# Optimization experiments

Hardware: AMD Instinct MI355X
Metric: run time of the kernel (lower is better)

The kernel has to match this reference:

```python
import jax, jax.numpy as jnp
import numpy as np

N_EMBED = 384
NUM_HEADS = 6
HEAD_SIZE = 64
B, T = 128, 256


def setup_inputs() -> dict:
    key = jax.random.key(0)
    ks = jax.random.split(key, 6)
    x = jax.random.normal(ks[0], (B, T, N_EMBED), dtype=jnp.float32)
    s = 0.02
    Wq = jax.random.normal(ks[1], (NUM_HEADS, N_EMBED, HEAD_SIZE), dtype=jnp.float32) * s
    Wk = jax.random.normal(ks[2], (NUM_HEADS, N_EMBED, HEAD_SIZE), dtype=jnp.float32) * s
    Wv = jax.random.normal(ks[3], (NUM_HEADS, N_EMBED, HEAD_SIZE), dtype=jnp.float32) * s
    Wp = jax.random.normal(ks[4], (NUM_HEADS * HEAD_SIZE, N_EMBED), dtype=jnp.float32) * s
    bp = jnp.zeros((N_EMBED,), dtype=jnp.float32)
    return {"x": x, "Wq": Wq, "Wk": Wk, "Wv": Wv, "Wp": Wp, "bp": bp}


def reference(x, Wq, Wk, Wv, Wp, bp):
    # x: [B,T,C]; Wq/Wk/Wv: [H,C,hs]; Wp: [H*hs, C]
    Bx, Tx, C = x.shape
    q = jnp.einsum('btc,hcd->bhtd', x, Wq)
    k = jnp.einsum('btc,hcd->bhtd', x, Wk)
    v = jnp.einsum('btc,hcd->bhtd', x, Wv)
    scale = HEAD_SIZE ** (-0.5)
    scores = jnp.einsum('bhtd,bhsd->bhts', q, k) * scale  # [B,H,T,T]
    causal = jnp.tril(jnp.ones((Tx, Tx), dtype=bool))
    scores = jnp.where(causal, scores, -jnp.inf)
    attn = jax.nn.softmax(scores, axis=-1)
    # dropout is identity in eval mode
    out = jnp.einsum('bhts,bhsd->bhtd', attn, v)  # [B,H,T,hs]
    out = out.transpose(0, 2, 1, 3).reshape(Bx, Tx, NUM_HEADS * HEAD_SIZE)
    return out @ Wp + bp
```

## Files before the change

### kernel.cpp

```cpp
#include <hip/hip_runtime.h>
#include <hip/hip_bf16.h>

#define C_DIM 384
#define H_NUM 6
#define HS    64
#define B_DIM 128
#define T_DIM 256
#define NROWS (B_DIM * T_DIM)

typedef unsigned short u16;
typedef unsigned int u32;
typedef short bf16x8 __attribute__((ext_vector_type(8)));
typedef float floatx4 __attribute__((ext_vector_type(4)));

__device__ __forceinline__ u16 f2b(float f) {
  __hip_bfloat16 h = __float2bfloat16(f);
  u16 u;
  __builtin_memcpy(&u, &h, 2);
  return u;
}
__device__ __forceinline__ void gload_lds16(const void* g, void* lds) {
  __builtin_amdgcn_global_load_lds(
      (const __attribute__((address_space(1))) u32*)g,
      (__attribute__((address_space(3))) u32*)lds, 16, 0, 0);
}

__global__ __launch_bounds__(256) void prep_kernel(
    const float* __restrict__ x, const float* __restrict__ Wq,
    const float* __restrict__ Wk, const float* __restrict__ Wv,
    const float* __restrict__ Wp, u16* __restrict__ xb,
    u16* __restrict__ Wh, u16* __restrict__ Wpt) {
  const int bid = blockIdx.x;
  const int tid = threadIdx.x;
  if (bid < 6144) {
    const int i = bid * 256 + tid;
    const int row = (i * 8) / C_DIM;
    const int c8 = (i * 8) % C_DIM;
    const float* p = x + (size_t)i * 8;
    const float4 f0 = *(const float4*)p;
    const float4 f1 = *(const float4*)(p + 4);
    bf16x8 pk;
    pk[0] = (short)f2b(f0.x); pk[1] = (short)f2b(f0.y);
    pk[2] = (short)f2b(f0.z); pk[3] = (short)f2b(f0.w);
    pk[4] = (short)f2b(f1.x); pk[5] = (short)f2b(f1.y);
    pk[6] = (short)f2b(f1.z); pk[7] = (short)f2b(f1.w);
    const int cd = c8 ^ ((row & 7) << 3);
    ((bf16x8*)xb)[(row * C_DIM + cd) >> 3] = pk;
  } else {
    const int idx = (bid - 6144) * 256 + tid;
    const int WHN = H_NUM * 192 * C_DIM;
    if (idx < WHN) {
      int h = idx / (192 * C_DIM);
      int rem = idx % (192 * C_DIM);
      int r = rem / C_DIM, c = rem % C_DIM;
      int tz = r >> 6, d = r & 63;
      const int cs = c ^ ((r & 7) << 3);
      const float* W = (tz == 0) ? Wq : (tz == 1) ? Wk : Wv;
      Wh[idx] = f2b(W[((size_t)h * C_DIM + cs) * HS + d]);
    } else {
      int j = idx - WHN;
      int n = j / C_DIM, c = j % C_DIM;
      const int cs = c ^ ((n & 7) << 3);
      Wpt[j] = f2b(Wp[cs * C_DIM + n]);
    }
  }
}

#define AS0_OFF 0
#define AS1_OFF 16384
#define BS0_OFF 32768
#define BS1_OFF 45056
#define QS_OFF  0
#define KLS_OFF 16384
#define VTS_OFF 32768
#define PLS_OFF 49152

template <bool DIAG>
__device__ __forceinline__ void attn_chunk_f(int c, int mt, int lane, int ln,
                                             int qd, const bf16x8* qf,
                                             const u16* smem, u16* Pw,
                                             floatx4* oacc, float* lsum) {
  floatx4 sacc[4];
#pragma unroll
  for (int st = 0; st < 4; ++st) {
    sacc[st] = floatx4{0.f, 0.f, 0.f, 0.f};
#pragma unroll
    for (int kc = 0; kc < 2; ++kc) {
      bf16x8 kf = *(const bf16x8*)&smem[KLS_OFF + ((c * 4 + st) * 2 + kc) * 512 +
                                        lane * 8];
      sacc[st] =
          __builtin_amdgcn_mfma_f32_16x16x32_bf16(qf[kc], kf, sacc[st], 0, 0, 0);
    }
  }
#pragma unroll
  for (int st = 0; st < 4; ++st) {
#pragma unroll
    for (int r = 0; r < 4; ++r) {
      const float sv = sacc[st][r] * 0.125f;
      float p = __expf(sv);
      if (DIAG) {
        const bool ok = (c * 64 + st * 16 + ln) <= (mt * 16 + qd * 4 + r);
        p = ok ? p : 0.f;
      }
      lsum[r] += p;
      Pw[(qd * 4 + r) * 72 + st * 16 + ln] = f2b(p);
    }
  }
#pragma unroll
  for (int kc2 = 0; kc2 < 2; ++kc2) {
    bf16x8 pf = *(const bf16x8*)&Pw[ln * 72 + kc2 * 32 + qd * 8];
#pragma unroll
    for (int dt = 0; dt < 4; ++dt) {
      bf16x8 vf = *(const bf16x8*)&smem[VTS_OFF + (dt * 16 + ln) * 256 +
                                        ((c * 64 + kc2 * 32 + qd * 8) ^
                                         ((ln & 7) << 3))];
      oacc[dt] =
          __builtin_amdgcn_mfma_f32_16x16x32_bf16(pf, vf, oacc[dt], 0, 0, 0);
    }
  }
}

__global__ __launch_bounds__(512) void qkv_attn_fused(
    const u16* __restrict__ xb, const u16* __restrict__ Wh,
    u16* __restrict__ y) {
  __shared__ __align__(16) u16 smem[58368];
  const int b = blockIdx.x;
  const int h = blockIdx.y;
  const u16* a_rows = xb + (size_t)b * 256 * C_DIM;
  const u16* wbase = Wh + (size_t)h * 192 * C_DIM;

  const int tid = threadIdx.x;
  const int lane = tid & 63;
  const int w = tid >> 6;
  const int lr = lane >> 3;
  const int lkc = (lane & 7) * 8;
  const int qd = lane >> 4;
  const int ln = lane & 15;
  const int sx = (ln & 7) << 3;
  const int wm = (w >> 1) * 64;
  const int wn = (w & 1) * 96;

  floatx4 acc[4][6];
#pragma unroll
  for (int i = 0; i < 4; ++i)
#pragma unroll
    for (int j = 0; j < 6; ++j) acc[i][j] = floatx4{0.f, 0.f, 0.f, 0.f};

#pragma unroll
  for (int s = 0; s < 4; ++s) {
    const int rbase = (s * 8 + w) * 8;
    gload_lds16(a_rows + (size_t)(rbase + lr) * C_DIM + lkc,
                smem + AS0_OFF + rbase * 64);
  }
#pragma unroll
  for (int s = 0; s < 3; ++s) {
    const int rbase = (s * 8 + w) * 8;
    gload_lds16(wbase + (size_t)(rbase + lr) * C_DIM + lkc,
                smem + BS0_OFF + rbase * 64);
  }

  for (int kb = 0; kb < 6; ++kb) {
    const int pa = (kb & 1) ? AS1_OFF : AS0_OFF;
    const int pb = (kb & 1) ? BS1_OFF : BS0_OFF;
    if (kb < 5) {
      const int qa = (kb & 1) ? AS0_OFF : AS1_OFF;
      const int qb = (kb & 1) ? BS0_OFF : BS1_OFF;
      const int k0 = (kb + 1) * 64;
#pragma unroll
      for (int s = 0; s < 4; ++s) {
        const int rbase = (s * 8 + w) * 8;
        gload_lds16(a_rows + (size_t)(rbase + lr) * C_DIM + k0 + lkc,
                    smem + qa + rbase * 64);
      }
#pragma unroll
      for (int s = 0; s < 3; ++s) {
        const int rbase = (s * 8 + w) * 8;
        gload_lds16(wbase + (size_t)(rbase + lr) * C_DIM + k0 + lkc,
                    smem + qb + rbase * 64);
      }
      asm volatile("s_waitcnt vmcnt(7)" ::: "memory");
    } else {
      asm volatile("s_waitcnt vmcnt(0)" ::: "memory");
    }
    __builtin_amdgcn_s_barrier();
    __builtin_amdgcn_sched_barrier(0);

#pragma unroll
    for (int kk = 0; kk < 2; ++kk) {
      bf16x8 af[4], bf[6];
#pragma unroll
      for (int mt = 0; mt < 4; ++mt)
        af[mt] = *(const bf16x8*)&smem[pa + (wm + mt * 16 + ln) * 64 +
                                       ((kk * 32 + qd * 8) ^ sx)];
#pragma unroll
      for (int nt = 0; nt < 6; ++nt)
        bf[nt] = *(const bf16x8*)&smem[pb + (wn + nt * 16 + ln) * 64 +
                                       ((kk * 32 + qd * 8) ^ sx)];
#pragma unroll
      for (int mt = 0; mt < 4; ++mt)
#pragma unroll
        for (int nt = 0; nt < 6; ++nt)
          acc[mt][nt] = __builtin_amdgcn_mfma_f32_16x16x32_bf16(
              af[mt], bf[nt], acc[mt][nt], 0, 0, 0);
    }
    __builtin_amdgcn_sched_barrier(0);
    __builtin_amdgcn_s_barrier();
  }

#pragma unroll
  for (int nt = 0; nt < 6; ++nt) {
    const int c0 = wn + nt * 16;
#pragma unroll
    for (int mt = 0; mt < 4; ++mt) {
#pragma unroll
      for (int r = 0; r < 4; ++r) {
        const int t = wm + mt * 16 + qd * 4 + r;
        const u16 val = f2b(acc[mt][nt][r]);
        if (c0 < 64) {
          smem[QS_OFF + t * 64 + c0 + ln] = val;
        } else if (c0 < 128) {
          const int d = c0 - 64 + ln;
          smem[KLS_OFF + ((t >> 4) << 10) + ((d >> 5) << 9) +
               (((d >> 3) & 3) << 7) + ((t & 15) << 3) + (d & 7)] = val;
        } else {
          const int dv = c0 - 128 + ln;
          smem[VTS_OFF + dv * 256 + (t ^ ((dv & 7) << 3))] = val;
        }
      }
    }
  }
  __syncthreads();

  u16* Pw = smem + PLS_OFF + w * 1152;
#pragma unroll
  for (int i = 0; i < 2; ++i) {
    const int mt = i ? (15 - w) : w;
    bf16x8 qf[2];
#pragma unroll
    for (int kc = 0; kc < 2; ++kc)
      qf[kc] = *(const bf16x8*)&smem[QS_OFF + (mt * 16 + ln) * 64 + kc * 32 +
                                     qd * 8];

    floatx4 oacc[4];
    float lsum[4];
#pragma unroll
    for (int dt = 0; dt < 4; ++dt) oacc[dt] = floatx4{0.f, 0.f, 0.f, 0.f};
#pragma unroll
    for (int r = 0; r < 4; ++r) lsum[r] = 0.f;

    const int cmax = mt >> 2;
    for (int c = 0; c < cmax; ++c)
      attn_chunk_f<false>(c, mt, lane, ln, qd, qf, smem, Pw, oacc, lsum);
    attn_chunk_f<true>(cmax, mt, lane, ln, qd, qf, smem, Pw, oacc, lsum);

#pragma unroll
    for (int off = 1; off < 16; off <<= 1)
#pragma unroll
      for (int r = 0; r < 4; ++r) lsum[r] += __shfl_xor(lsum[r], off);

#pragma unroll
    for (int r = 0; r < 4; ++r) {
      const float inv = 1.f / lsum[r];
      const int t = mt * 16 + qd * 4 + r;
      const int sy = (t & 7) << 3;
      u16* yo = y + ((size_t)b * T_DIM + t) * C_DIM + h * HS;
#pragma unroll
      for (int dt = 0; dt < 4; ++dt)
        yo[(dt * 16 + ln) ^ sy] = f2b(oacc[dt][r] * inv);
    }
  }
}

#define PAS0 0
#define PAS1 8192
#define PBS0 16384
#define PBS1 24576

__global__ __launch_bounds__(256) void proj_gemm(
    const u16* __restrict__ yb, const u16* __restrict__ Wpt,
    const float* __restrict__ bp, float* __restrict__ out) {
  __shared__ __align__(16) u16 smem[33792];
  const int row0 = blockIdx.x * 128;
  const int n0 = blockIdx.y * 128;
  const u16* a_rows = yb + (size_t)row0 * C_DIM;
  const u16* bt_rows = Wpt + (size_t)n0 * C_DIM;

  const int tid = threadIdx.x;
  const int lane = tid & 63;
  const int w = tid >> 6;
  const int lr = lane >> 3;
  const int lkc = (lane & 7) * 8;
  const int qd = lane >> 4;
  const int ln = lane & 15;
  const int sx = (ln & 7) << 3;
  const int mw = (w >> 1) * 64;
  const int nw = (w & 1) * 64;

  floatx4 acc[4][4];
#pragma unroll
  for (int i = 0; i < 4; ++i)
#pragma unroll
    for (int j = 0; j < 4; ++j) acc[i][j] = floatx4{0.f, 0.f, 0.f, 0.f};

#pragma unroll
  for (int s = 0; s < 4; ++s) {
    const int rbase = (s * 4 + w) * 8;
    gload_lds16(a_rows + (size_t)(rbase + lr) * C_DIM + lkc,
                smem + PAS0 + rbase * 64);
    gload_lds16(bt_rows + (size_t)(rbase + lr) * C_DIM + lkc,
                smem + PBS0 + rbase * 64);
  }

  for (int kb = 0; kb < 6; ++kb) {
    const int pa = (kb & 1) ? PAS1 : PAS0;
    const int pb = (kb & 1) ? PBS1 : PBS0;
    if (kb < 5) {
      const int qa = (kb & 1) ? PAS0 : PAS1;
      const int qb = (kb & 1) ? PBS0 : PBS1;
      const int k0 = (kb + 1) * 64;
#pragma unroll
      for (int s = 0; s < 4; ++s) {
        const int rbase = (s * 4 + w) * 8;
        gload_lds16(a_rows + (size_t)(rbase + lr) * C_DIM + k0 + lkc,
                    smem + qa + rbase * 64);
        gload_lds16(bt_rows + (size_t)(rbase + lr) * C_DIM + k0 + lkc,
                    smem + qb + rbase * 64);
      }
      asm volatile("s_waitcnt vmcnt(8)" ::: "memory");
    } else {
      asm volatile("s_waitcnt vmcnt(0)" ::: "memory");
    }
    __builtin_amdgcn_s_barrier();
    __builtin_amdgcn_sched_barrier(0);

#pragma unroll
    for (int kk = 0; kk < 2; ++kk) {
      bf16x8 af[4], bf[4];
#pragma unroll
      for (int mt = 0; mt < 4; ++mt)
        af[mt] = *(const bf16x8*)&smem[pa + (mw + mt * 16 + ln) * 64 +
                                       ((kk * 32 + qd * 8) ^ sx)];
#pragma unroll
      for (int nt = 0; nt < 4; ++nt)
        bf[nt] = *(const bf16x8*)&smem[pb + (nw + nt * 16 + ln) * 64 +
                                       ((kk * 32 + qd * 8) ^ sx)];
#pragma unroll
      for (int mt = 0; mt < 4; ++mt)
#pragma unroll
        for (int nt = 0; nt < 4; ++nt)
          acc[mt][nt] = __builtin_amdgcn_mfma_f32_16x16x32_bf16(
              af[mt], bf[nt], acc[mt][nt], 0, 0, 0);
    }
    __builtin_amdgcn_sched_barrier(0);
    __builtin_amdgcn_s_barrier();
  }

  float* Osf = (float*)smem;
#pragma unroll
  for (int nt = 0; nt < 4; ++nt) {
#pragma unroll
    for (int mt = 0; mt < 4; ++mt) {
#pragma unroll
      for (int r = 0; r < 4; ++r) {
        Osf[(mw + mt * 16 + qd * 4 + r) * 132 + nw + nt * 16 + ln] =
            acc[mt][nt][r];
      }
    }
  }
  __syncthreads();
#pragma unroll
  for (int it = 0; it < 16; ++it) {
    const int idx = it * 1024 + tid * 4;
    const int lrow = idx >> 7, lcol = idx & 127;
    const float4 o = *(const float4*)&Osf[lrow * 132 + lcol];
    const float4 bb = *(const float4*)&bp[n0 + lcol];
    const float4 res{o.x + bb.x, o.y + bb.y, o.z + bb.z, o.w + bb.w};
    *(float4*)&out[(size_t)(row0 + lrow) * C_DIM + n0 + lcol] = res;
  }
}

extern "C" void kernel_launch(void* const* d_in, const int* in_sizes, int n_in,
                              void* d_out, int out_size, void* d_ws, size_t ws_size,
                              hipStream_t stream) {
  const float* x  = (const float*)d_in[0];
  const float* Wq = (const float*)d_in[1];
  const float* Wk = (const float*)d_in[2];
  const float* Wv = (const float*)d_in[3];
  const float* Wp = (const float*)d_in[4];
  const float* bp = (const float*)d_in[5];
  float* out = (float*)d_out;

  const size_t n_x = (size_t)NROWS * C_DIM;

  u16* Wh  = (u16*)d_ws;
  u16* Wpt = Wh + (size_t)H_NUM * 192 * C_DIM;
  u16* xb  = Wpt + C_DIM * C_DIM;
  u16* y   = xb + n_x;

  prep_kernel<<<6144 + 2304, 256, 0, stream>>>(x, Wq, Wk, Wv, Wp, xb, Wh, Wpt);
  qkv_attn_fused<<<dim3(B_DIM, H_NUM), 512, 0, stream>>>(xb, Wh, y);
  proj_gemm<<<dim3(NROWS / 128, 3), 256, 0, stream>>>(y, Wpt, bp, out);
}
```

Measured before the change: 182.8 us.

## Fuse output projection into attention kernel via last-head-arrives counter

Removes the separate projection GEMM launch. Each attention block increments a per-batch atomic counter after writing its head output, and the last of the six head blocks for a batch computes the full 256x384 projection for that batch, including the bias add, writing floats directly without LDS staging. This saves a kernel launch and lets projection overlap with other batches' attention, but the projection work is done serially by only 128 blocks at the tail and output stores are uncoalesced per-lane scalar writes.

```diff
diff --git a/kernel.cpp b/kernel.cpp
--- a/kernel.cpp
+++ b/kernel.cpp
@@ -29,7 +29,7 @@
     const float* __restrict__ x, const float* __restrict__ Wq,
     const float* __restrict__ Wk, const float* __restrict__ Wv,
     const float* __restrict__ Wp, u16* __restrict__ xb,
-    u16* __restrict__ Wh, u16* __restrict__ Wpt) {
+    u16* __restrict__ Wh, u16* __restrict__ Wpt, u32* __restrict__ cnt) {
   const int bid = blockIdx.x;
   const int tid = threadIdx.x;
   if (bid < 6144) {
@@ -48,6 +48,7 @@
     ((bf16x8*)xb)[(row * C_DIM + cd) >> 3] = pk;
   } else {
     const int idx = (bid - 6144) * 256 + tid;
+    if (bid == 6144 && tid < B_DIM) cnt[tid] = 0;
     const int WHN = H_NUM * 192 * C_DIM;
     if (idx < WHN) {
       int h = idx / (192 * C_DIM);
@@ -74,6 +75,11 @@
 #define KLS_OFF 16384
 #define VTS_OFF 32768
 #define PLS_OFF 49152
+#define PA0_OFF 0
+#define PA1_OFF 16384
+#define PB0_OFF 32768
+#define PB1_OFF 40960
+#define FLAG_OFF 49152
 
 template <bool DIAG>
 __device__ __forceinline__ void attn_chunk_f(int c, int mt, int lane, int ln,
@@ -122,7 +128,8 @@
 
 __global__ __launch_bounds__(512) void qkv_attn_fused(
     const u16* __restrict__ xb, const u16* __restrict__ Wh,
-    u16* __restrict__ y) {
+    const u16* __restrict__ Wpt, const float* __restrict__ bp,
+    u16* __restrict__ y, float* __restrict__ out, u32* __restrict__ cnt) {
   __shared__ __align__(16) u16 smem[58368];
   const int b = blockIdx.x;
   const int h = blockIdx.y;
@@ -269,113 +276,105 @@
         yo[(dt * 16 + ln) ^ sy] = f2b(oacc[dt][r] * inv);
     }
   }
-}
-
-#define PAS0 0
-#define PAS1 8192
-#define PBS0 16384
-#define PBS1 24576
-
-__global__ __launch_bounds__(256) void proj_gemm(
-    const u16* __restrict__ yb, const u16* __restrict__ Wpt,
-    const float* __restrict__ bp, float* __restrict__ out) {
-  __shared__ __align__(16) u16 smem[33792];
-  const int row0 = blockIdx.x * 128;
-  const int n0 = blockIdx.y * 128;
-  const u16* a_rows = yb + (size_t)row0 * C_DIM;
-  const u16* bt_rows = Wpt + (size_t)n0 * C_DIM;
-
-  const int tid = threadIdx.x;
-  const int lane = tid & 63;
-  const int w = tid >> 6;
-  const int lr = lane >> 3;
-  const int lkc = (lane & 7) * 8;
-  const int qd = lane >> 4;
-  const int ln = lane & 15;
-  const int sx = (ln & 7) << 3;
-  const int mw = (w >> 1) * 64;
-  const int nw = (w & 1) * 64;
-
-  floatx4 acc[4][4];
-#pragma unroll
-  for (int i = 0; i < 4; ++i)
-#pragma unroll
-    for (int j = 0; j < 4; ++j) acc[i][j] = floatx4{0.f, 0.f, 0.f, 0.f};
-
-#pragma unroll
-  for (int s = 0; s < 4; ++s) {
-    const int rbase = (s * 4 + w) * 8;
-    gload_lds16(a_rows + (size_t)(rbase + lr) * C_DIM + lkc,
-                smem + PAS0 + rbase * 64);
-    gload_lds16(bt_rows + (size_t)(rbase + lr) * C_DIM + lkc,
-                smem + PBS0 + rbase * 64);
-  }
-
-  for (int kb = 0; kb < 6; ++kb) {
-    const int pa = (kb & 1) ? PAS1 : PAS0;
-    const int pb = (kb & 1) ? PBS1 : PBS0;
-    if (kb < 5) {
-      const int qa = (kb & 1) ? PAS0 : PAS1;
-      const int qb = (kb & 1) ? PBS0 : PBS1;
-      const int k0 = (kb + 1) * 64;
-#pragma unroll
-      for (int s = 0; s < 4; ++s) {
-        const int rbase = (s * 4 + w) * 8;
-        gload_lds16(a_rows + (size_t)(rbase + lr) * C_DIM + k0 + lkc,
-                    smem + qa + rbase * 64);
-        gload_lds16(bt_rows + (size_t)(rbase + lr) * C_DIM + k0 + lkc,
-                    smem + qb + rbase * 64);
-      }
-      asm volatile("s_waitcnt vmcnt(8)" ::: "memory");
-    } else {
-      asm volatile("s_waitcnt vmcnt(0)" ::: "memory");
-    }
-    __builtin_amdgcn_s_barrier();
-    __builtin_amdgcn_sched_barrier(0);
-
-#pragma unroll
-    for (int kk = 0; kk < 2; ++kk) {
-      bf16x8 af[4], bf[4];
-#pragma unroll
-      for (int mt = 0; mt < 4; ++mt)
-        af[mt] = *(const bf16x8*)&smem[pa + (mw + mt * 16 + ln) * 64 +
-                                       ((kk * 32 + qd * 8) ^ sx)];
-#pragma unroll
-      for (int nt = 0; nt < 4; ++nt)
-        bf[nt] = *(const bf16x8*)&smem[pb + (nw + nt * 16 + ln) * 64 +
-                                       ((kk * 32 + qd * 8) ^ sx)];
-#pragma unroll
-      for (int mt = 0; mt < 4; ++mt)
+
+  __threadfence();
+  __syncthreads();
+  volatile int* flag = (volatile int*)(smem + FLAG_OFF);
+  if (tid == 0) {
+    const u32 old = atomicAdd(&cnt[b], 1u);
+    *flag = (old == 5u) ? 1 : 0;
+  }
+  __syncthreads();
+  if (*flag == 0) return;
+  __threadfence();
+
+  const u16* yb_rows = y + (size_t)b * T_DIM * C_DIM;
+  const int nwp = (w & 1) * 64;
+
+  for (int pn = 0; pn < 3; ++pn) {
+    const int n0 = pn * 128;
+    const u16* bt_rows = Wpt + (size_t)n0 * C_DIM;
+
+    floatx4 pacc[4][4];
+#pragma unroll
+    for (int i = 0; i < 4; ++i)
+#pragma unroll
+      for (int j = 0; j < 4; ++j) pacc[i][j] = floatx4{0.f, 0.f, 0.f, 0.f};
+
+#pragma unroll
+    for (int s = 0; s < 4; ++s) {
+      const int rbase = (s * 8 + w) * 8;
+      gload_lds16(yb_rows + (size_t)(rbase + lr) * C_DIM + lkc,
+                  smem + PA0_OFF + rbase * 64);
+    }
+#pragma unroll
+    for (int s = 0; s < 2; ++s) {
+      const int rbase = (s * 8 + w) * 8;
+      gload_lds16(bt_rows + (size_t)(rbase + lr) * C_DIM + lkc,
+                  smem + PB0_OFF + rbase * 64);
+    }
+
+    for (int kb = 0; kb < 6; ++kb) {
+      const int pa = (kb & 1) ? PA1_OFF : PA0_OFF;
+      const int pb = (kb & 1) ? PB1_OFF : PB0_OFF;
+      if (kb < 5) {
+        const int qa = (kb & 1) ? PA0_OFF : PA1_OFF;
+        const int qb = (kb & 1) ? PB0_OFF : PB1_OFF;
+        const int k0 = (kb + 1) * 64;
+#pragma unroll
+        for (int s = 0; s < 4; ++s) {
+          const int rbase = (s * 8 + w) * 8;
+          gload_lds16(yb_rows + (size_t)(rbase + lr) * C_DIM + k0 + lkc,
+                      smem + qa + rbase * 64);
+        }
+#pragma unroll
+        for (int s = 0; s < 2; ++s) {
+          const int rbase = (s * 8 + w) * 8;
+          gload_lds16(bt_rows + (size_t)(rbase + lr) * C_DIM + k0 + lkc,
+                      smem + qb + rbase * 64);
+        }
+        asm volatile("s_waitcnt vmcnt(6)" ::: "memory");
+      } else {
+        asm volatile("s_waitcnt vmcnt(0)" ::: "memory");
+      }
+      __builtin_amdgcn_s_barrier();
+      __builtin_amdgcn_sched_barrier(0);
+
+#pragma unroll
+      for (int kk = 0; kk < 2; ++kk) {
+        bf16x8 af[4], bf[4];
+#pragma unroll
+        for (int mt = 0; mt < 4; ++mt)
+          af[mt] = *(const bf16x8*)&smem[pa + (wm + mt * 16 + ln) * 64 +
+                                         ((kk * 32 + qd * 8) ^ sx)];
 #pragma unroll
         for (int nt = 0; nt < 4; ++nt)
-          acc[mt][nt] = __builtin_amdgcn_mfma_f32_16x16x32_bf16(
-              af[mt], bf[nt], acc[mt][nt], 0, 0, 0);
-    }
-    __builtin_amdgcn_sched_barrier(0);
-    __builtin_amdgcn_s_barrier();
-  }
-
-  float* Osf = (float*)smem;
-#pragma unroll
-  for (int nt = 0; nt < 4; ++nt) {
-#pragma unroll
-    for (int mt = 0; mt < 4; ++mt) {
-#pragma unroll
-      for (int r = 0; r < 4; ++r) {
-        Osf[(mw + mt * 16 + qd * 4 + r) * 132 + nw + nt * 16 + ln] =
-            acc[mt][nt][r];
-      }
-    }
-  }
-  __syncthreads();
-#pragma unroll
-  for (int it = 0; it < 16; ++it) {
-    const int idx = it * 1024 + tid * 4;
-    const int lrow = idx >> 7, lcol = idx & 127;
-    const float4 o = *(const float4*)&Osf[lrow * 132 + lcol];
-    const float4 bb = *(const float4*)&bp[n0 + lcol];
-    const float4 res{o.x + bb.x, o.y + bb.y, o.z + bb.z, o.w + bb.w};
-    *(float4*)&out[(size_t)(row0 + lrow) * C_DIM + n0 + lcol] = res;
+          bf[nt] = *(const bf16x8*)&smem[pb + (nwp + nt * 16 + ln) * 64 +
+                                         ((kk * 32 + qd * 8) ^ sx)];
+#pragma unroll
+        for (int mt = 0; mt < 4; ++mt)
+#pragma unroll
+          for (int nt = 0; nt < 4; ++nt)
+            pacc[mt][nt] = __builtin_amdgcn_mfma_f32_16x16x32_bf16(
+                af[mt], bf[nt], pacc[mt][nt], 0, 0, 0);
+      }
+      __builtin_amdgcn_sched_barrier(0);
+      __builtin_amdgcn_s_barrier();
+    }
+
+#pragma unroll
+    for (int nt = 0; nt < 4; ++nt) {
+      const int col = n0 + nwp + nt * 16 + ln;
+      const float bias = bp[col];
+#pragma unroll
+      for (int mt = 0; mt < 4; ++mt) {
+#pragma unroll
+        for (int r = 0; r < 4; ++r) {
+          const int grow = b * T_DIM + wm + mt * 16 + qd * 4 + r;
+          out[(size_t)grow * C_DIM + col] = pacc[mt][nt][r] + bias;
+        }
+      }
+    }
   }
 }
 
@@ -396,8 +395,10 @@
   u16* Wpt = Wh + (size_t)H_NUM * 192 * C_DIM;
   u16* xb  = Wpt + C_DIM * C_DIM;
   u16* y   = xb + n_x;
-
-  prep_kernel<<<6144 + 2304, 256, 0, stream>>>(x, Wq, Wk, Wv, Wp, xb, Wh, Wpt);
-  qkv_attn_fused<<<dim3(B_DIM, H_NUM), 512, 0, stream>>>(xb, Wh, y);
-  proj_gemm<<<dim3(NROWS / 128, 3), 256, 0, stream>>>(y, Wpt, bp, out);
-}
+  u32* cnt = (u32*)(y + n_x);
+
+  prep_kernel<<<6144 + 2304, 256, 0, stream>>>(x, Wq, Wk, Wv, Wp, xb, Wh, Wpt,
+                                               cnt);
+  qkv_attn_fused<<<dim3(B_DIM, H_NUM), 512, 0, stream>>>(xb, Wh, Wpt, bp, y,
+                                                         out, cnt);
+}
```

Measured after the change: 383.9 us. +109.9%, slower.

## Fuse fp32-to-bf16 conversion of x into the QKV attention kernel

Applied to the files above, without the earlier changes.

The separate pass that converts x to a swizzled bf16 buffer is removed. The fused QKV/attention kernel now loads fp32 x tiles into registers, converts them, and writes them to LDS itself. The weight-only prep kernel is kept. This saves a full write and re-read of the bf16 copy of x and one launch's worth of work. In exchange, each of the six head blocks per batch reads fp32 x, doubling the bytes per read, and the A operand moves from async global-to-LDS loads to register staging with plain __syncthreads, which may reduce load/compute overlap.

```diff
diff --git a/kernel.cpp b/kernel.cpp
--- a/kernel.cpp
+++ b/kernel.cpp
@@ -25,44 +25,25 @@
       (__attribute__((address_space(3))) u32*)lds, 16, 0, 0);
 }
 
-__global__ __launch_bounds__(256) void prep_kernel(
-    const float* __restrict__ x, const float* __restrict__ Wq,
-    const float* __restrict__ Wk, const float* __restrict__ Wv,
-    const float* __restrict__ Wp, u16* __restrict__ xb,
+__global__ __launch_bounds__(256) void prep_w(
+    const float* __restrict__ Wq, const float* __restrict__ Wk,
+    const float* __restrict__ Wv, const float* __restrict__ Wp,
     u16* __restrict__ Wh, u16* __restrict__ Wpt) {
-  const int bid = blockIdx.x;
-  const int tid = threadIdx.x;
-  if (bid < 6144) {
-    const int i = bid * 256 + tid;
-    const int row = (i * 8) / C_DIM;
-    const int c8 = (i * 8) % C_DIM;
-    const float* p = x + (size_t)i * 8;
-    const float4 f0 = *(const float4*)p;
-    const float4 f1 = *(const float4*)(p + 4);
-    bf16x8 pk;
-    pk[0] = (short)f2b(f0.x); pk[1] = (short)f2b(f0.y);
-    pk[2] = (short)f2b(f0.z); pk[3] = (short)f2b(f0.w);
-    pk[4] = (short)f2b(f1.x); pk[5] = (short)f2b(f1.y);
-    pk[6] = (short)f2b(f1.z); pk[7] = (short)f2b(f1.w);
-    const int cd = c8 ^ ((row & 7) << 3);
-    ((bf16x8*)xb)[(row * C_DIM + cd) >> 3] = pk;
+  const int idx = blockIdx.x * 256 + threadIdx.x;
+  const int WHN = H_NUM * 192 * C_DIM;
+  if (idx < WHN) {
+    int h = idx / (192 * C_DIM);
+    int rem = idx % (192 * C_DIM);
+    int r = rem / C_DIM, c = rem % C_DIM;
+    int tz = r >> 6, d = r & 63;
+    const int cs = c ^ ((r & 7) << 3);
+    const float* W = (tz == 0) ? Wq : (tz == 1) ? Wk : Wv;
+    Wh[idx] = f2b(W[((size_t)h * C_DIM + cs) * HS + d]);
   } else {
-    const int idx = (bid - 6144) * 256 + tid;
-    const int WHN = H_NUM * 192 * C_DIM;
-    if (idx < WHN) {
-      int h = idx / (192 * C_DIM);
-      int rem = idx % (192 * C_DIM);
-      int r = rem / C_DIM, c = rem % C_DIM;
-      int tz = r >> 6, d = r & 63;
-      const int cs = c ^ ((r & 7) << 3);
-      const float* W = (tz == 0) ? Wq : (tz == 1) ? Wk : Wv;
-      Wh[idx] = f2b(W[((size_t)h * C_DIM + cs) * HS + d]);
-    } else {
-      int j = idx - WHN;
-      int n = j / C_DIM, c = j % C_DIM;
-      const int cs = c ^ ((n & 7) << 3);
-      Wpt[j] = f2b(Wp[cs * C_DIM + n]);
-    }
+    int j = idx - WHN;
+    int n = j / C_DIM, c = j % C_DIM;
+    const int cs = c ^ ((n & 7) << 3);
+    Wpt[j] = f2b(Wp[cs * C_DIM + n]);
   }
 }
 
@@ -120,13 +101,42 @@
   }
 }
 
+#define A_ISSUE(K0)                                                     \
+  {                                                                     \
+    _Pragma("unroll") for (int u = 0; u < 4; ++u) {                     \
+      const int idx_ = u * 512 + tid;                                   \
+      const int row_ = idx_ >> 3, c8_ = (idx_ & 7) * 8;                 \
+      const float* p_ = xg + (size_t)row_ * C_DIM + (K0) + c8_;         \
+      ar[2 * u] = *(const float4*)p_;                                   \
+      ar[2 * u + 1] = *(const float4*)(p_ + 4);                         \
+    }                                                                   \
+  }
+#define A_WRITE(DST)                                                    \
+  {                                                                     \
+    _Pragma("unroll") for (int u = 0; u < 4; ++u) {                     \
+      const int idx_ = u * 512 + tid;                                   \
+      const int row_ = idx_ >> 3, c8_ = (idx_ & 7) * 8;                 \
+      bf16x8 pk;                                                        \
+      pk[0] = (short)f2b(ar[2 * u].x);                                  \
+      pk[1] = (short)f2b(ar[2 * u].y);                                  \
+      pk[2] = (short)f2b(ar[2 * u].z);                                  \
+      pk[3] = (short)f2b(ar[2 * u].w);                                  \
+      pk[4] = (short)f2b(ar[2 * u + 1].x);                              \
+      pk[5] = (short)f2b(ar[2 * u + 1].y);                              \
+      pk[6] = (short)f2b(ar[2 * u + 1].z);                              \
+      pk[7] = (short)f2b(ar[2 * u + 1].w);                              \
+      *(bf16x8*)&smem[(DST) + row_ * 64 +                               \
+                      (c8_ ^ ((row_ & 7) << 3))] = pk;                  \
+    }                                                                   \
+  }
+
 __global__ __launch_bounds__(512) void qkv_attn_fused(
-    const u16* __restrict__ xb, const u16* __restrict__ Wh,
+    const float* __restrict__ x, const u16* __restrict__ Wh,
     u16* __restrict__ y) {
   __shared__ __align__(16) u16 smem[58368];
   const int b = blockIdx.x;
   const int h = blockIdx.y;
-  const u16* a_rows = xb + (size_t)b * 256 * C_DIM;
+  const float* xg = x + (size_t)b * 256 * C_DIM;
   const u16* wbase = Wh + (size_t)h * 192 * C_DIM;
 
   const int tid = threadIdx.x;
@@ -146,44 +156,33 @@
 #pragma unroll
     for (int j = 0; j < 6; ++j) acc[i][j] = floatx4{0.f, 0.f, 0.f, 0.f};
 
-#pragma unroll
-  for (int s = 0; s < 4; ++s) {
-    const int rbase = (s * 8 + w) * 8;
-    gload_lds16(a_rows + (size_t)(rbase + lr) * C_DIM + lkc,
-                smem + AS0_OFF + rbase * 64);
-  }
+  float4 ar[8];
+
+  A_ISSUE(0);
 #pragma unroll
   for (int s = 0; s < 3; ++s) {
     const int rbase = (s * 8 + w) * 8;
     gload_lds16(wbase + (size_t)(rbase + lr) * C_DIM + lkc,
                 smem + BS0_OFF + rbase * 64);
   }
+  A_WRITE(AS0_OFF);
+  __syncthreads();
 
   for (int kb = 0; kb < 6; ++kb) {
     const int pa = (kb & 1) ? AS1_OFF : AS0_OFF;
     const int pb = (kb & 1) ? BS1_OFF : BS0_OFF;
+    const int qa = (kb & 1) ? AS0_OFF : AS1_OFF;
+    const int qb = (kb & 1) ? BS0_OFF : BS1_OFF;
     if (kb < 5) {
-      const int qa = (kb & 1) ? AS0_OFF : AS1_OFF;
-      const int qb = (kb & 1) ? BS0_OFF : BS1_OFF;
       const int k0 = (kb + 1) * 64;
-#pragma unroll
-      for (int s = 0; s < 4; ++s) {
-        const int rbase = (s * 8 + w) * 8;
-        gload_lds16(a_rows + (size_t)(rbase + lr) * C_DIM + k0 + lkc,
-                    smem + qa + rbase * 64);
-      }
+      A_ISSUE(k0);
 #pragma unroll
       for (int s = 0; s < 3; ++s) {
         const int rbase = (s * 8 + w) * 8;
         gload_lds16(wbase + (size_t)(rbase + lr) * C_DIM + k0 + lkc,
                     smem + qb + rbase * 64);
       }
-      asm volatile("s_waitcnt vmcnt(7)" ::: "memory");
-    } else {
-      asm volatile("s_waitcnt vmcnt(0)" ::: "memory");
-    }
-    __builtin_amdgcn_s_barrier();
-    __builtin_amdgcn_sched_barrier(0);
+    }
 
 #pragma unroll
     for (int kk = 0; kk < 2; ++kk) {
@@ -203,8 +202,9 @@
           acc[mt][nt] = __builtin_amdgcn_mfma_f32_16x16x32_bf16(
               af[mt], bf[nt], acc[mt][nt], 0, 0, 0);
     }
-    __builtin_amdgcn_sched_barrier(0);
-    __builtin_amdgcn_s_barrier();
+
+    if (kb < 5) A_WRITE(qa);
+    __syncthreads();
   }
 
 #pragma unroll
@@ -390,14 +390,11 @@
   const float* bp = (const float*)d_in[5];
   float* out = (float*)d_out;
 
-  const size_t n_x = (size_t)NROWS * C_DIM;
-
   u16* Wh  = (u16*)d_ws;
   u16* Wpt = Wh + (size_t)H_NUM * 192 * C_DIM;
-  u16* xb  = Wpt + C_DIM * C_DIM;
-  u16* y   = xb + n_x;
-
-  prep_kernel<<<6144 + 2304, 256, 0, stream>>>(x, Wq, Wk, Wv, Wp, xb, Wh, Wpt);
-  qkv_attn_fused<<<dim3(B_DIM, H_NUM), 512, 0, stream>>>(xb, Wh, y);
+  u16* y   = Wpt + C_DIM * C_DIM;
+
+  prep_w<<<2304, 256, 0, stream>>>(Wq, Wk, Wv, Wp, Wh, Wpt);
+  qkv_attn_fused<<<dim3(B_DIM, H_NUM), 512, 0, stream>>>(x, Wh, y);
   proj_gemm<<<dim3(NROWS / 128, 3), 256, 0, stream>>>(y, Wpt, bp, out);
 }
```

After: 187.0 us. 2.3% more time.
